# Kernel tuning notes

Hardware: AMD Instinct MI355X
Metric: run time of the kernel (lower is better)

The kernel has to match this reference:

```python
import jax, jax.numpy as jnp
import numpy as np

TEMPERATURE = 0.1
MAX_POS = 6
MAX_NEG = 30
POS_NEG_RATIO = 1.0
NEG_K = max(6, MAX_NEG)  # static top-k width for negatives


def setup_inputs() -> dict:
    key = jax.random.key(0)
    k1, k2 = jax.random.split(key)
    K, D = 8192, 256
    features = jax.random.normal(k1, (K, D), dtype=jnp.float32)
    labels = jax.random.randint(k2, (K,), 0, 64, dtype=jnp.int64)
    return {"features": features, "labels": labels}


def reference(features, labels):
    K = features.shape[0]
    # L2-normalize embeddings (F.normalize, dim=1)
    f = features / jnp.clip(jnp.linalg.norm(features, axis=1, keepdims=True), 1e-12)
    sim = jnp.matmul(f, f.T) / TEMPERATURE                      # [K, K]
    sim = sim - jax.lax.stop_gradient(jnp.max(sim, axis=1, keepdims=True))
    exp_sim = jnp.exp(sim)

    eye = jnp.eye(K, dtype=bool)
    same = labels[:, None] == labels[None, :]
    mask_pos = same & ~eye                                      # same label, off-diagonal
    mask_neg = ~same                                            # 1 - mask_pos - eye

    n_pos = jnp.sum(mask_pos, axis=1).astype(jnp.int32)         # [K]
    n_neg = jnp.sum(mask_neg, axis=1).astype(jnp.int32)         # [K]

    # per-anchor dynamic sample counts (vectorized version of the python loop)
    max_pos_i = jnp.minimum(
        n_pos,
        jnp.maximum(1, jnp.minimum(MAX_POS, (n_neg.astype(jnp.float32) * POS_NEG_RATIO).astype(jnp.int32))),
    )
    max_neg_i = jnp.minimum(n_neg, NEG_K)
    valid_row = (n_pos > 0) & (n_neg > 0)
    max_pos_i = jnp.where(valid_row, max_pos_i, 0)
    max_neg_i = jnp.where(valid_row, max_neg_i, 0)

    rows = jnp.arange(K)[:, None]
    neg_inf = jnp.finfo(sim.dtype).min

    # top-k hard positives by similarity, masked to the first max_pos_i ranks
    pos_scores = jnp.where(mask_pos, sim, neg_inf)
    _, pos_idx = jax.lax.top_k(pos_scores, MAX_POS)             # [K, MAX_POS]
    pos_keep = (jnp.arange(MAX_POS)[None, :] < max_pos_i[:, None]).astype(sim.dtype)
    new_mask_pos = jnp.zeros((K, K), sim.dtype).at[rows, pos_idx].add(pos_keep)

    # random negatives: randperm emulated by top-k of uniform scores over neg slots
    rand = jax.random.uniform(jax.random.key(42), (K, K), dtype=jnp.float32)
    neg_scores = jnp.where(mask_neg, rand, -1.0)
    _, neg_idx = jax.lax.top_k(neg_scores, NEG_K)               # [K, NEG_K]
    neg_keep = (jnp.arange(NEG_K)[None, :] < max_neg_i[:, None]).astype(sim.dtype)
    new_mask_neg = jnp.zeros((K, K), sim.dtype).at[rows, neg_idx].add(neg_keep)

    numerator = jnp.sum(exp_sim * new_mask_pos, axis=1)
    denominator = jnp.sum(exp_sim * (new_mask_pos + new_mask_neg), axis=1)
    loss = -jnp.log(jnp.clip(numerator / denominator, 1e-8))
    return jnp.mean(loss)
```

## Files before the change

### kernel.cpp

```cpp
#include <hip/hip_runtime.h>
#include <hip/hip_fp16.h>
#include <math.h>
#include <stdint.h>


#define NEGK 30
#define MAXP 6
#define MAXBC 320
#define RGB 32
#define CGB 64

typedef _Float16 h2v __attribute__((ext_vector_type(2)));

__device__ __forceinline__ uint64_t mix64(uint64_t z) {
  z += 0x9E3779B97F4A7C15ULL;
  z = (z ^ (z >> 30)) * 0xBF58476D1CE4E5B9ULL;
  z = (z ^ (z >> 27)) * 0x94D049BB133111EBULL;
  return z ^ (z >> 31);
}

__device__ __forceinline__ float wave_reduce_add(float p) {
#pragma unroll
  for (int o = 32; o; o >>= 1) p += __shfl_down(p, o, 64);
  return p;
}

__device__ __forceinline__ float dot8h(uint4 a, uint4 b, float acc) {
  const h2v* pa = (const h2v*)&a;
  const h2v* pb = (const h2v*)&b;
#if __has_builtin(__builtin_amdgcn_fdot2)
#pragma unroll
  for (int q = 0; q < 4; ++q) acc = __builtin_amdgcn_fdot2(pa[q], pb[q], acc, false);
#else
#pragma unroll
  for (int q = 0; q < 4; ++q)
    acc += (float)pa[q].x * (float)pb[q].x + (float)pa[q].y * (float)pb[q].y;
#endif
  return acc;
}

__global__ __launch_bounds__(256) void k_prep(const float* __restrict__ F,
                                              const int* __restrict__ labels, int K,
                                              __half* __restrict__ Fh,
                                              int* __restrict__ g_start,
                                              int* __restrict__ g_soff,
                                              int* __restrict__ g_bucket,
                                              int4* __restrict__ g_meta) {
  __shared__ int cnt[64], start[65], cur[64], soff_s[64];
  const int tid = threadIdx.x;

  if ((int)blockIdx.x < K / 4) {
    const int row = blockIdx.x * 4 + (tid >> 6);
    const int lane = tid & 63;
    const float4 a = ((const float4*)(F + (size_t)row * 256))[lane];
    float p = a.x * a.x + a.y * a.y + a.z * a.z + a.w * a.w;
    p = wave_reduce_add(p);
    p = __shfl(p, 0, 64);
    const float inv = 1.0f / fmaxf(sqrtf(p), 1e-12f);
    union { __half2 h[2]; uint2 u; } cv;
    cv.h[0] = __float22half2_rn(make_float2(a.x * inv, a.y * inv));
    cv.h[1] = __float22half2_rn(make_float2(a.z * inv, a.w * inv));
    ((uint2*)(Fh + (size_t)row * 256))[lane] = cv.u;
    return;
  }

  if (tid < 64) cnt[tid] = 0;
  __syncthreads();
  for (int t = tid; t < K; t += 256) atomicAdd(&cnt[labels[t] & 63], 1);
  __syncthreads();
  if (tid == 0) {
    int acc = 0, sacc = 0;
    for (int l = 0; l < 64; ++l) {
      start[l] = acc;
      const int B = cnt[l];
      acc += B;
      soff_s[l] = sacc;
      const int Bc = B < MAXBC ? B : MAXBC;
      sacc += Bc * Bc;
    }
    start[64] = acc;
  }
  __syncthreads();
  if (tid < 64) { cur[tid] = start[tid]; g_soff[tid] = soff_s[tid]; }
  if (tid < 65) g_start[tid] = start[tid];
  __syncthreads();
  for (int t = tid; t < K; t += 256) {
    const int l = labels[t] & 63;
    const int p = atomicAdd(&cur[l], 1);
    g_bucket[p] = t;
    g_meta[t] = make_int4(start[l], cnt[l], p - start[l], soff_s[l]);
  }
}

__global__ __launch_bounds__(256) void k_gram(const __half* __restrict__ Fh,
                                              const int* __restrict__ g_start,
                                              const int* __restrict__ g_soff,
                                              const int* __restrict__ g_bucket,
                                              float* __restrict__ g_sims) {
  __shared__ uint4 sA[RGB * 32];

  const int b  = blockIdx.x;
  const int bs = g_start[b];
  const int B  = g_start[b + 1] - bs;
  const int Bc = B < MAXBC ? B : MAXBC;
  const int r0 = blockIdx.y * RGB;
  const int c0 = blockIdx.z * CGB;
  if (r0 >= Bc || c0 >= Bc) return;
  const int tid = threadIdx.x;

  for (int u = tid; u < RGB * 32; u += 256) {
    const int r = u >> 5, c = u & 31;
    const int rr = r0 + r;
    const int gr = g_bucket[bs + (rr < Bc ? rr : Bc - 1)];
    sA[u] = ((const uint4*)(Fh + (size_t)gr * 256))[c];
  }
  __syncthreads();

  const int wv = tid >> 6, lane = tid & 63;
  const int cc = c0 + lane;
  const int gq = g_bucket[bs + (cc < Bc ? cc : Bc - 1)];
  const uint4* fq = (const uint4*)(Fh + (size_t)gq * 256);
  const uint4* sw = sA + wv * 8 * 32;

  float acc[8];
#pragma unroll
  for (int r = 0; r < 8; ++r) acc[r] = 0.0f;

  for (int k = 0; k < 32; k += 4) {
    const uint4 a0 = fq[k], a1 = fq[k + 1], a2 = fq[k + 2], a3 = fq[k + 3];
#pragma unroll
    for (int r = 0; r < 8; ++r) {
      float t = acc[r];
      t = dot8h(sw[r * 32 + k    ], a0, t);
      t = dot8h(sw[r * 32 + k + 1], a1, t);
      t = dot8h(sw[r * 32 + k + 2], a2, t);
      t = dot8h(sw[r * 32 + k + 3], a3, t);
      acc[r] = t;
    }
  }

  if (cc < Bc) {
    float* outb = g_sims + g_soff[b];
#pragma unroll
    for (int r = 0; r < 8; ++r) {
      const int rr = r0 + wv * 8 + r;
      if (rr < Bc)
        outb[(size_t)rr * Bc + cc] = (rr == cc) ? -3.0e38f : acc[r] * 10.0f;
    }
  }
}

__global__ __launch_bounds__(256) void k_anchor(
    const __half* __restrict__ Fh, const int* __restrict__ g_bucket,
    const int4* __restrict__ g_meta, const float* __restrict__ g_sims,
    float* __restrict__ g_part, int K) {
  __shared__ uint4 sA[4 * 32];
  const int wv = threadIdx.x >> 6;
  const int lane = threadIdx.x & 63;
  const int i = blockIdx.x * 4 + wv;

  ((uint2*)sA)[wv * 64 + lane] = ((const uint2*)(Fh + (size_t)i * 256))[lane];
  const uint4* sw = sA + wv * 32;

  const int4 mt = g_meta[i];
  const int bs = mt.x, B = mt.y;
  const int Bc = B < MAXBC ? B : MAXBC;
  int loc = mt.z;
  if (loc >= Bc) loc = 0;
  const int n_pos = B - 1;
  const int n_neg = K - B;
  const float* simrow = g_sims + mt.w + (size_t)loc * Bc;

  float v[5];
#pragma unroll
  for (int rr = 0; rr < 5; ++rr) {
    const int t = lane + rr * 64;
    v[rr] = (t < Bc) ? simrow[t] : -3.4e38f;
  }

  int t6 = n_neg < MAXP ? n_neg : MAXP;
  if (t6 < 1) t6 = 1;
  int take = n_pos < t6 ? n_pos : t6;
  if (n_pos <= 0 || n_neg <= 0) take = 0;
  const int target = (take > 0) ? (n_neg < NEGK ? n_neg : NEGK) : 0;

  const int s = lane & 3, g = lane >> 2;
  const int n0 = g, n1 = 16 + g;
  const uint64_t z0 = mix64(((uint64_t)(uint32_t)i << 32) | (uint32_t)n0);
  const uint64_t z1 = mix64(((uint64_t)(uint32_t)i << 32) | (uint32_t)n1);
  const unsigned int r0 = (unsigned int)(((uint64_t)(uint32_t)z0 * (uint64_t)n_neg) >> 32);
  const unsigned int r1 = (unsigned int)(((uint64_t)(uint32_t)z1 * (uint64_t)n_neg) >> 32);
  const int pos0 = (r0 < (unsigned int)bs) ? (int)r0 : (int)r0 + B;
  const int pos1 = (r1 < (unsigned int)bs) ? (int)r1 : (int)r1 + B;
  const bool pv0 = (n0 < target), pv1 = (n1 < target);
  const int j0 = pv0 ? g_bucket[pos0] : 0;
  const int j1 = pv1 ? g_bucket[pos1] : 0;
  const uint4* f0 = (const uint4*)(Fh + (size_t)j0 * 256);
  const uint4* f1 = (const uint4*)(Fh + (size_t)j1 * 256);
  float d0 = 0.0f, d1 = 0.0f;
#pragma unroll
  for (int k = 0; k < 8; ++k) {
    const uint4 aw = sw[k * 4 + s];
    d0 = dot8h(f0[k * 4 + s], aw, d0);
    d1 = dot8h(f1[k * 4 + s], aw, d1);
  }
  d0 += __shfl_xor(d0, 1, 64); d0 += __shfl_xor(d0, 2, 64);
  d1 += __shfl_xor(d1, 1, 64); d1 += __shfl_xor(d1, 2, 64);
  float e = 0.0f;
  if (s == 0) {
    if (pv0) e += expf(d0 * 10.0f);
    if (pv1) e += expf(d1 * 10.0f);
  }
  const float wsum = wave_reduce_add(e);

  float num = 0.0f;
  for (int r = 0; r < take; ++r) {
    float best = v[0];
#pragma unroll
    for (int c = 1; c < 5; ++c) best = fmaxf(best, v[c]);
#pragma unroll
    for (int o = 1; o < 64; o <<= 1) best = fmaxf(best, __shfl_xor(best, o, 64));
    num += expf(best);
#pragma unroll
    for (int c = 0; c < 5; ++c)
      if (v[c] == best) v[c] = -3.4e38f;
  }

  if (lane == 0) {
    float ls = 0.0f;
    if (take > 0) {
      const float denom = num + wsum;
      float ratio = denom > 0.0f ? num / denom : 0.0f;
      ratio = fmaxf(ratio, 1e-8f);
      ls = -logf(ratio);
    }
    g_part[i] = ls;
  }
}

__global__ __launch_bounds__(1024) void k_final(const float* __restrict__ g_part,
                                                float* __restrict__ out, int K) {
  __shared__ float s[16];
  float p = 0.0f;
  for (int t = threadIdx.x; t < K; t += 1024) p += g_part[t];
  p = wave_reduce_add(p);
  if ((threadIdx.x & 63) == 0) s[threadIdx.x >> 6] = p;
  __syncthreads();
  if (threadIdx.x == 0) {
    float tot = 0.0f;
#pragma unroll
    for (int w = 0; w < 16; ++w) tot += s[w];
    out[0] = tot / (float)K;
  }
}

extern "C" void kernel_launch(void* const* d_in, const int* in_sizes, int n_in,
                              void* d_out, int out_size, void* d_ws, size_t ws_size,
                              hipStream_t stream) {
  (void)n_in; (void)out_size; (void)ws_size;
  const float* F = (const float*)d_in[0];
  const int* labels = (const int*)d_in[1];
  const int K = in_sizes[1];
  float* out = (float*)d_out;

  char* ws = (char*)d_ws;
  size_t off = 0;
  int*   g_start  = (int*)(ws + off);   off += 512;
  int*   g_soff   = (int*)(ws + off);   off += 256;
  int*   g_bucket = (int*)(ws + off);   off += (size_t)K * 4;
  float* g_part   = (float*)(ws + off); off += (size_t)K * 4;
  off = (off + 255) & ~(size_t)255;
  int4*  g_meta   = (int4*)(ws + off);  off += (size_t)K * 16;
  __half* Fh      = (__half*)(ws + off); off += (size_t)K * 256 * 2;
  float* g_sims   = (float*)(ws + off);  off += (size_t)MAXBC * K * 4;

  k_prep<<<K / 4 + 1, 256, 0, stream>>>(F, labels, K, Fh, g_start, g_soff,
                                        g_bucket, g_meta);
  {
    dim3 grid(64, (MAXBC + RGB - 1) / RGB, (MAXBC + CGB - 1) / CGB);
    k_gram<<<grid, 256, 0, stream>>>(Fh, g_start, g_soff, g_bucket, g_sims);
  }
  k_anchor<<<K / 4, 256, 0, stream>>>(Fh, g_bucket, g_meta, g_sims, g_part, K);
  k_final<<<1, 1024, 0, stream>>>(g_part, out, K);
}
```

Before: 115.8 us.

## Compute per-label Gram tiles with MFMA 32x32x16 and swizzled LDS staging

Replaces the scalar fdot2-based per-bucket Gram kernel with a 64x64-tile kernel where each wave computes a 32x32 block using the MFMA f32_32x32x16_f16 instruction. Both row and column feature tiles are staged in shared memory with an XOR swizzle to avoid bank conflicts, and the grid changes to match the new square tile size. This targets the ALU-bound dot-product loop in the similarity stage. The Gram kernel is only one of several stages, so any benefit to the total is limited, and the larger LDS footprint may reduce occupancy.

```diff
diff --git a/kernel.cpp b/kernel.cpp
--- a/kernel.cpp
+++ b/kernel.cpp
@@ -7,10 +7,11 @@
 #define NEGK 30
 #define MAXP 6
 #define MAXBC 320
-#define RGB 32
-#define CGB 64
+#define GT 64
 
 typedef _Float16 h2v __attribute__((ext_vector_type(2)));
+typedef _Float16 f16x8 __attribute__((ext_vector_type(8)));
+typedef float f32x16 __attribute__((ext_vector_type(16)));
 
 __device__ __forceinline__ uint64_t mix64(uint64_t z) {
   z += 0x9E3779B97F4A7C15ULL;
@@ -97,56 +98,59 @@
                                               const int* __restrict__ g_soff,
                                               const int* __restrict__ g_bucket,
                                               float* __restrict__ g_sims) {
-  __shared__ uint4 sA[RGB * 32];
+  __shared__ uint4 sR[64 * 32];
+  __shared__ uint4 sC[64 * 32];
 
   const int b  = blockIdx.x;
   const int bs = g_start[b];
   const int B  = g_start[b + 1] - bs;
   const int Bc = B < MAXBC ? B : MAXBC;
-  const int r0 = blockIdx.y * RGB;
-  const int c0 = blockIdx.z * CGB;
+  if (Bc <= 0) return;
+  const int r0 = blockIdx.y * GT;
+  const int c0 = blockIdx.z * GT;
   if (r0 >= Bc || c0 >= Bc) return;
   const int tid = threadIdx.x;
 
-  for (int u = tid; u < RGB * 32; u += 256) {
-    const int r = u >> 5, c = u & 31;
+  for (int u = tid; u < 64 * 32; u += 256) {
+    const int r = u >> 5, ch = u & 31;
+    const int sl = ch ^ (r & 31);
     const int rr = r0 + r;
     const int gr = g_bucket[bs + (rr < Bc ? rr : Bc - 1)];
-    sA[u] = ((const uint4*)(Fh + (size_t)gr * 256))[c];
+    sR[(r << 5) | sl] = ((const uint4*)(Fh + (size_t)gr * 256))[ch];
+    const int cc = c0 + r;
+    const int gc = g_bucket[bs + (cc < Bc ? cc : Bc - 1)];
+    sC[(r << 5) | sl] = ((const uint4*)(Fh + (size_t)gc * 256))[ch];
   }
   __syncthreads();
 
   const int wv = tid >> 6, lane = tid & 63;
-  const int cc = c0 + lane;
-  const int gq = g_bucket[bs + (cc < Bc ? cc : Bc - 1)];
-  const uint4* fq = (const uint4*)(Fh + (size_t)gq * 256);
-  const uint4* sw = sA + wv * 8 * 32;
-
-  float acc[8];
-#pragma unroll
-  for (int r = 0; r < 8; ++r) acc[r] = 0.0f;
-
-  for (int k = 0; k < 32; k += 4) {
-    const uint4 a0 = fq[k], a1 = fq[k + 1], a2 = fq[k + 2], a3 = fq[k + 3];
-#pragma unroll
-    for (int r = 0; r < 8; ++r) {
-      float t = acc[r];
-      t = dot8h(sw[r * 32 + k    ], a0, t);
-      t = dot8h(sw[r * 32 + k + 1], a1, t);
-      t = dot8h(sw[r * 32 + k + 2], a2, t);
-      t = dot8h(sw[r * 32 + k + 3], a3, t);
-      acc[r] = t;
-    }
-  }
-
-  if (cc < Bc) {
-    float* outb = g_sims + g_soff[b];
-#pragma unroll
-    for (int r = 0; r < 8; ++r) {
-      const int rr = r0 + wv * 8 + r;
-      if (rr < Bc)
-        outb[(size_t)rr * Bc + cc] = (rr == cc) ? -3.0e38f : acc[r] * 10.0f;
-    }
+  const int wr = (wv >> 1) * 32;
+  const int wc = (wv & 1) * 32;
+  const int rA = wr + (lane & 31);
+  const int rB = wc + (lane & 31);
+  const int kq = lane >> 5;
+
+  f32x16 acc;
+#pragma unroll
+  for (int q = 0; q < 16; ++q) acc[q] = 0.0f;
+
+#pragma unroll
+  for (int it = 0; it < 16; ++it) {
+    const int slot = 2 * it + kq;
+    const f16x8 a  = *(const f16x8*)&sR[(rA << 5) | (slot ^ (rA & 31))];
+    const f16x8 bf = *(const f16x8*)&sC[(rB << 5) | (slot ^ (rB & 31))];
+    acc = __builtin_amdgcn_mfma_f32_32x32x16_f16(a, bf, acc, 0, 0, 0);
+  }
+
+  float* outb = g_sims + g_soff[b];
+  const int ccs = c0 + wc + (lane & 31);
+  const bool cok = ccs < Bc;
+#pragma unroll
+  for (int reg = 0; reg < 16; ++reg) {
+    const int row = (reg & 3) + 8 * (reg >> 2) + 4 * (lane >> 5);
+    const int rrs = r0 + wr + row;
+    if (cok && rrs < Bc)
+      outb[(size_t)rrs * Bc + ccs] = (rrs == ccs) ? -3.0e38f : acc[reg] * 10.0f;
   }
 }
 
@@ -277,7 +281,7 @@
   k_prep<<<K / 4 + 1, 256, 0, stream>>>(F, labels, K, Fh, g_start, g_soff,
                                         g_bucket, g_meta);
   {
-    dim3 grid(64, (MAXBC + RGB - 1) / RGB, (MAXBC + CGB - 1) / CGB);
+    dim3 grid(64, (MAXBC + GT - 1) / GT, (MAXBC + GT - 1) / GT);
     k_gram<<<grid, 256, 0, stream>>>(Fh, g_start, g_soff, g_bucket, g_sims);
   }
   k_anchor<<<K / 4, 256, 0, stream>>>(Fh, g_bucket, g_meta, g_sims, g_part, K);
```

Result: faster. 105.1 us (-9.3%).
